# Kernel optimization log

Hardware: AMD Instinct MI355X
Metric: run time of the kernel (lower is better)

Reference implementation:

```python
import jax, jax.numpy as jnp
import numpy as np

IN_F = 4096
OUT_F = 4096
RANK = 32
GROUP = 64  # int4 weight quantization group size along in_features


def setup_inputs() -> dict:
    key = jax.random.key(0)
    k_x, k_w, k_s, k_ld, k_lu, k_b = jax.random.split(key, 6)
    x = jax.random.normal(k_x, (4096, IN_F), dtype=jnp.float32)
    # int4 weight codes in [-8, 7], stored as int32
    qweight = jax.random.randint(k_w, (OUT_F, IN_F), -8, 8, dtype=jnp.int32)
    # per-(out_channel, group) scales
    wscale = jax.random.uniform(k_s, (OUT_F, IN_F // GROUP), dtype=jnp.float32, minval=0.01, maxval=0.05)
    # low-rank SVD correction branch (LoRA-style)
    lora_down = jax.random.normal(k_ld, (RANK, IN_F), dtype=jnp.float32) * 0.02
    lora_up = jax.random.normal(k_lu, (OUT_F, RANK), dtype=jnp.float32) * 0.02
    bias = jax.random.normal(k_b, (OUT_F,), dtype=jnp.float32) * 0.01
    return {"x": x, "qweight": qweight, "wscale": wscale,
            "lora_down": lora_down, "lora_up": lora_up, "bias": bias}


def reference(x, qweight, wscale, lora_down, lora_up, bias):
    out_f, in_f = qweight.shape
    # dequantize int4 weights group-wise: W[o, g*G+i] = q * scale[o, g]
    W = (qweight.astype(jnp.float32).reshape(out_f, in_f // GROUP, GROUP)
         * wscale[:, :, None]).reshape(out_f, in_f)
    # per-token symmetric int4 activation quantization (W4A4 main path)
    ascale = jnp.maximum(jnp.max(jnp.abs(x), axis=-1, keepdims=True), 1e-6) / 7.0
    xq = jnp.clip(jnp.round(x / ascale), -8.0, 7.0) * ascale  # fake-quantized x
    # main quantized GEMM
    main = jnp.einsum('ti,oi->to', xq, W)
    # low-rank correction uses full-precision activations
    lora = jnp.einsum('tr,or->to', jnp.einsum('ti,ri->tr', x, lora_down), lora_up)
    return main + lora + bias[None, :]
```

## Files before the change

### kernel.cpp

```cpp
#include <hip/hip_runtime.h>

typedef __bf16 bf16x8 __attribute__((ext_vector_type(8)));
typedef float f32x4 __attribute__((ext_vector_type(4)));
typedef unsigned short u16;

#define IN_F 4096
#define OUT_F 4096
#define NTOK 4096
#define RANK 32
#define KEXT 4160
#define NT (KEXT / 64)
#define ROWB ((size_t)KEXT * 2)

__device__ __forceinline__ u16 f2bf(float f) {
  union { float f; unsigned u; } c; c.f = f;
  unsigned u = c.u;
  return (u16)((u + 0x7FFFu + ((u >> 16) & 1u)) >> 16);
}

__device__ __forceinline__ void gload_lds16(const void* g, void* l) {
  __builtin_amdgcn_global_load_lds((const __attribute__((address_space(1))) void*)g,
                                   (__attribute__((address_space(3))) void*)l,
                                   16, 0, 0);
}

__global__ __launch_bounds__(256) void prep_kernel(const float* __restrict__ x,
                                                   u16* __restrict__ A,
                                                   float* __restrict__ ascale) {
  int t = blockIdx.x;
  int tid = threadIdx.x;
  const float4* xr = (const float4*)(x + (size_t)t * IN_F);
  float4 v[4];
  float m = 0.f;
#pragma unroll
  for (int i = 0; i < 4; ++i) {
    v[i] = xr[tid + i * 256];
    m = fmaxf(m, fmaxf(fmaxf(fabsf(v[i].x), fabsf(v[i].y)),
                       fmaxf(fabsf(v[i].z), fabsf(v[i].w))));
  }
#pragma unroll
  for (int off = 32; off > 0; off >>= 1) m = fmaxf(m, __shfl_xor(m, off));
  __shared__ float wmax[4];
  if ((tid & 63) == 0) wmax[tid >> 6] = m;
  __syncthreads();
  m = fmaxf(fmaxf(wmax[0], wmax[1]), fmaxf(wmax[2], wmax[3]));
  float as = fmaxf(m, 1e-6f) / 7.f;
  float inv = 1.f / as;
  if (tid == 0) ascale[t] = as;
  u16* Ar = A + (size_t)t * KEXT;
#pragma unroll
  for (int i = 0; i < 4; ++i) {
    float q0 = fminf(fmaxf(rintf(v[i].x * inv), -8.f), 7.f);
    float q1 = fminf(fmaxf(rintf(v[i].y * inv), -8.f), 7.f);
    float q2 = fminf(fmaxf(rintf(v[i].z * inv), -8.f), 7.f);
    float q3 = fminf(fmaxf(rintf(v[i].w * inv), -8.f), 7.f);
    ushort4 u;
    u.x = f2bf(q0); u.y = f2bf(q1); u.z = f2bf(q2); u.w = f2bf(q3);
    *(ushort4*)(Ar + (size_t)(tid + i * 256) * 4) = u;
  }
  if (tid < 8) {
    ushort4 z; z.x = z.y = z.z = z.w = 0;
    *(ushort4*)(Ar + IN_F + 32 + tid * 4) = z;
  }
}

__global__ __launch_bounds__(256) void dequant_kernel(const int* __restrict__ qw,
                                                      const float* __restrict__ wscale,
                                                      const float* __restrict__ lu,
                                                      u16* __restrict__ B) {
  int o = blockIdx.x;
  int tid = threadIdx.x;
  const int4* qr = (const int4*)(qw + (size_t)o * IN_F);
  const float* sr = wscale + (size_t)o * (IN_F / 64);
  u16* Br = B + (size_t)o * KEXT;
#pragma unroll
  for (int s = 0; s < 4; ++s) {
    int e = tid + s * 256;
    int4 q = qr[e];
    float sc = sr[e >> 4];
    ushort4 u;
    u.x = f2bf((float)q.x * sc);
    u.y = f2bf((float)q.y * sc);
    u.z = f2bf((float)q.z * sc);
    u.w = f2bf((float)q.w * sc);
    *(ushort4*)(Br + (size_t)4 * e) = u;
  }
  if (tid < RANK) Br[IN_F + tid] = f2bf(lu[(size_t)o * RANK + tid]);
  if (tid < 8) {
    ushort4 z; z.x = z.y = z.z = z.w = 0;
    *(ushort4*)(Br + IN_F + 32 + tid * 4) = z;
  }
}

__global__ __launch_bounds__(256) void lorad_kernel(const float* __restrict__ x,
                                                    const float* __restrict__ ld,
                                                    float* __restrict__ tr8) {
  __shared__ float Xs[128][68];
  __shared__ float Ls[32][68];
  int b = blockIdx.x;
  int t0 = (b >> 3) * 128;
  int kbase = (b & 7) * 512;
  int tid = threadIdx.x;
  int rb = tid & 7;
  int tb = tid >> 3;
  float acc[4][4];
#pragma unroll
  for (int i = 0; i < 4; ++i)
#pragma unroll
    for (int j = 0; j < 4; ++j) acc[i][j] = 0.f;

  for (int kc = 0; kc < 512; kc += 64) {
    int k0 = kbase + kc;
    __syncthreads();
#pragma unroll
    for (int s = 0; s < 8; ++s) {
      int e = tid + s * 256;
      int row = e >> 4, c4 = (e & 15) * 4;
      float4 vv = *(const float4*)(x + (size_t)(t0 + row) * IN_F + k0 + c4);
      *(float4*)&Xs[row][c4] = vv;
    }
#pragma unroll
    for (int s = 0; s < 2; ++s) {
      int e = tid + s * 256;
      int row = e >> 4, c4 = (e & 15) * 4;
      float4 vv = *(const float4*)(ld + (size_t)row * IN_F + k0 + c4);
      *(float4*)&Ls[row][c4] = vv;
    }
    __syncthreads();
    for (int k4 = 0; k4 < 64; k4 += 4) {
      float4 lv[4], xv[4];
#pragma unroll
      for (int r = 0; r < 4; ++r) lv[r] = *(float4*)&Ls[rb + r * 8][k4];
#pragma unroll
      for (int mm = 0; mm < 4; ++mm) xv[mm] = *(float4*)&Xs[tb + mm * 32][k4];
#pragma unroll
      for (int mm = 0; mm < 4; ++mm)
#pragma unroll
        for (int r = 0; r < 4; ++r)
          acc[mm][r] += xv[mm].x * lv[r].x + xv[mm].y * lv[r].y +
                        xv[mm].z * lv[r].z + xv[mm].w * lv[r].w;
    }
  }
  float* dst = tr8 + (size_t)(b & 7) * NTOK * RANK;
#pragma unroll
  for (int mm = 0; mm < 4; ++mm)
#pragma unroll
    for (int r = 0; r < 4; ++r)
      dst[(size_t)(t0 + tb + mm * 32) * RANK + rb + r * 8] = acc[mm][r];
}

__global__ __launch_bounds__(256) void trwrite_kernel(const float* __restrict__ tr8,
                                                      const float* __restrict__ ascale,
                                                      u16* __restrict__ A) {
  int idx = blockIdx.x * 256 + threadIdx.x;
  int t = idx >> 5, r = idx & 31;
  float s = 0.f;
#pragma unroll
  for (int k = 0; k < 8; ++k) s += tr8[(size_t)k * NTOK * RANK + idx];
  A[(size_t)t * KEXT + IN_F + r] = f2bf(s / ascale[t]);
}


__device__ __forceinline__ void stage_tile(const char* g, char* ldst, int tid) {
#pragma unroll
  for (int h = 0; h < 4; ++h)
    gload_lds16(g + (size_t)h * (64 * ROWB), ldst + h * 8192 + tid * 16);
}

#define BARRIER() do { asm volatile("s_barrier" ::: "memory"); __builtin_amdgcn_sched_barrier(0); } while (0)

__global__ __launch_bounds__(512, 2) void gemm_kernel(const u16* __restrict__ A,
                                                      const u16* __restrict__ B,
                                                      const float* __restrict__ ascale,
                                                      const float* __restrict__ bias,
                                                      float* __restrict__ out) {
  __shared__ __align__(16) char smem[131072];
  int b = blockIdx.x;
  int swz = (b & 7) * 32 + (b >> 3);
  int by = swz >> 4, bx = swz & 15;
  int tm = by * 256, tn = bx * 256;
  int tid = threadIdx.x;
  int lane = tid & 63, wid = tid >> 6;
  int wr = wid >> 2, wc = wid & 3;
  int l15 = lane & 15, l4 = lane >> 4;
  int xorb = (l15 & 7) << 4;
  int colx0 = (l4 * 16) ^ xorb;
  int colx1 = (l4 * 16 + 64) ^ xorb;
  int a_base = wr * 16384 + l15 * 128;
  int b_base = wc * 8192 + l15 * 128;

  int r0 = tid >> 3;
  int cb = (((tid & 7) ^ ((tid >> 3) & 7)) << 4);
  const char* ag = (const char*)A + (size_t)(tm + r0) * ROWB + cb;
  const char* bg = (const char*)B + (size_t)(tn + r0) * ROWB + cb;

  f32x4 acc[8][4];
#pragma unroll
  for (int i = 0; i < 8; ++i)
#pragma unroll
    for (int j = 0; j < 4; ++j) acc[i][j] = (f32x4){0.f, 0.f, 0.f, 0.f};

  stage_tile(ag, smem, tid);
  stage_tile(bg, smem + 65536, tid);
  stage_tile(ag + 128, smem + 32768, tid);
  stage_tile(bg + 128, smem + 65536 + 32768, tid);
  asm volatile("s_waitcnt vmcnt(8)" ::: "memory");
  BARRIER();

  const char* apf = ag + 256;
  const char* bpf = bg + 256;
  bf16x8 af[8][2], bf[2][2];

  for (int t = 0; t < NT; ++t) {
    int c = t & 1;
    int ao = c * 32768 + a_base;
    int bo = 65536 + c * 32768 + b_base;
    bool pf = (t + 2) < NT;

#pragma unroll
    for (int i = 0; i < 4; ++i) {
      af[i][0] = *(const bf16x8*)(smem + ao + i * 2048 + colx0);
      af[i][1] = *(const bf16x8*)(smem + ao + i * 2048 + colx1);
    }
#pragma unroll
    for (int j = 0; j < 2; ++j) {
      bf[j][0] = *(const bf16x8*)(smem + bo + j * 2048 + colx0);
      bf[j][1] = *(const bf16x8*)(smem + bo + j * 2048 + colx1);
    }
    BARRIER();
    __builtin_amdgcn_s_setprio(1);
#pragma unroll
    for (int i = 0; i < 4; ++i)
#pragma unroll
      for (int j = 0; j < 2; ++j) {
        acc[i][j] = __builtin_amdgcn_mfma_f32_16x16x32_bf16(af[i][0], bf[j][0], acc[i][j], 0, 0, 0);
        acc[i][j] = __builtin_amdgcn_mfma_f32_16x16x32_bf16(af[i][1], bf[j][1], acc[i][j], 0, 0, 0);
      }
    __builtin_amdgcn_s_setprio(0);
    __builtin_amdgcn_sched_barrier(0);
    BARRIER();

#pragma unroll
    for (int i = 4; i < 8; ++i) {
      af[i][0] = *(const bf16x8*)(smem + ao + i * 2048 + colx0);
      af[i][1] = *(const bf16x8*)(smem + ao + i * 2048 + colx1);
    }
    BARRIER();
    __builtin_amdgcn_s_setprio(1);
#pragma unroll
    for (int i = 4; i < 8; ++i)
#pragma unroll
      for (int j = 0; j < 2; ++j) {
        acc[i][j] = __builtin_amdgcn_mfma_f32_16x16x32_bf16(af[i][0], bf[j][0], acc[i][j], 0, 0, 0);
        acc[i][j] = __builtin_amdgcn_mfma_f32_16x16x32_bf16(af[i][1], bf[j][1], acc[i][j], 0, 0, 0);
      }
    __builtin_amdgcn_s_setprio(0);
    __builtin_amdgcn_sched_barrier(0);
    BARRIER();

#pragma unroll
    for (int j = 0; j < 2; ++j) {
      bf[j][0] = *(const bf16x8*)(smem + bo + (j + 2) * 2048 + colx0);
      bf[j][1] = *(const bf16x8*)(smem + bo + (j + 2) * 2048 + colx1);
    }
    if (pf) stage_tile(apf, smem + c * 32768, tid);
    BARRIER();
    __builtin_amdgcn_s_setprio(1);
#pragma unroll
    for (int i = 0; i < 4; ++i)
#pragma unroll
      for (int j = 0; j < 2; ++j) {
        acc[i][j + 2] = __builtin_amdgcn_mfma_f32_16x16x32_bf16(af[i][0], bf[j][0], acc[i][j + 2], 0, 0, 0);
        acc[i][j + 2] = __builtin_amdgcn_mfma_f32_16x16x32_bf16(af[i][1], bf[j][1], acc[i][j + 2], 0, 0, 0);
      }
    __builtin_amdgcn_s_setprio(0);
    __builtin_amdgcn_sched_barrier(0);
    BARRIER();

    if (pf) {
      stage_tile(bpf, smem + 65536 + c * 32768, tid);
      asm volatile("s_waitcnt vmcnt(8)" ::: "memory");
    } else if (t == NT - 2) {
      asm volatile("s_waitcnt vmcnt(0)" ::: "memory");
    }
    BARRIER();
    __builtin_amdgcn_s_setprio(1);
#pragma unroll
    for (int i = 4; i < 8; ++i)
#pragma unroll
      for (int j = 0; j < 2; ++j) {
        acc[i][j + 2] = __builtin_amdgcn_mfma_f32_16x16x32_bf16(af[i][0], bf[j][0], acc[i][j + 2], 0, 0, 0);
        acc[i][j + 2] = __builtin_amdgcn_mfma_f32_16x16x32_bf16(af[i][1], bf[j][1], acc[i][j + 2], 0, 0, 0);
      }
    __builtin_amdgcn_s_setprio(0);
    __builtin_amdgcn_sched_barrier(0);
    BARRIER();

    apf += 128;
    bpf += 128;
  }

#pragma unroll
  for (int i = 0; i < 8; ++i) {
    int rowb = tm + wr * 128 + i * 16 + l4 * 4;
#pragma unroll
    for (int j = 0; j < 4; ++j) {
      int col = tn + wc * 64 + j * 16 + l15;
      float bv = bias[col];
#pragma unroll
      for (int q = 0; q < 4; ++q)
        out[(size_t)(rowb + q) * OUT_F + col] = acc[i][j][q] * ascale[rowb + q] + bv;
    }
  }
}

extern "C" void kernel_launch(void* const* d_in, const int* in_sizes, int n_in,
                              void* d_out, int out_size, void* d_ws, size_t ws_size,
                              hipStream_t stream) {
  const float* x = (const float*)d_in[0];
  const int* qw = (const int*)d_in[1];
  const float* wscale = (const float*)d_in[2];
  const float* ld = (const float*)d_in[3];
  const float* lu = (const float*)d_in[4];
  const float* bias = (const float*)d_in[5];
  float* out = (float*)d_out;

  char* ws = (char*)d_ws;
  const size_t szA = (size_t)NTOK * KEXT * sizeof(u16);
  const size_t szB = (size_t)OUT_F * KEXT * sizeof(u16);
  u16* Aext = (u16*)ws;
  u16* Bext = (u16*)(ws + szA);
  float* ascale = (float*)(ws + szA + szB);
  float* tr8 = (float*)(ws + szA + szB + 16384);

  prep_kernel<<<NTOK, 256, 0, stream>>>(x, Aext, ascale);
  dequant_kernel<<<OUT_F, 256, 0, stream>>>(qw, wscale, lu, Bext);
  lorad_kernel<<<256, 256, 0, stream>>>(x, ld, tr8);
  trwrite_kernel<<<NTOK * RANK / 256, 256, 0, stream>>>(tr8, ascale, Aext);
  gemm_kernel<<<(NTOK / 256) * (OUT_F / 256), 512, 0, stream>>>(Aext, Bext, ascale, bias, out);
}
```

Before: 194.0 us.

## Hoist all LDS fragment loads to iteration start and cut barriers per K-step

Each K-step now reads all A and B fragments from LDS at the start, holding 8x2 A and 4x2 B vectors, instead of interleaving four load phases between the MFMA blocks. This cuts the workgroup barriers per iteration from about eight to three, placed only where global-to-LDS prefetches need buffer reuse to be safe. The aim is to remove barrier stalls and let the LDS reads overlap with MFMA work. In exchange, more fragment registers are live at once, which adds register pressure under the 512-thread, 2-block launch bounds and could cause spills or lower occupancy.

```diff
diff --git a/kernel.cpp b/kernel.cpp
--- a/kernel.cpp
+++ b/kernel.cpp
@@ -167,7 +167,8 @@
     gload_lds16(g + (size_t)h * (64 * ROWB), ldst + h * 8192 + tid * 16);
 }
 
-#define BARRIER() do { asm volatile("s_barrier" ::: "memory"); __builtin_amdgcn_sched_barrier(0); } while (0)
+#define PIN_BARRIER() do { __builtin_amdgcn_sched_barrier(0); \
+                           asm volatile("s_barrier" ::: "memory"); } while (0)
 
 __global__ __launch_bounds__(512, 2) void gemm_kernel(const u16* __restrict__ A,
                                                       const u16* __restrict__ B,
@@ -205,11 +206,11 @@
   stage_tile(ag + 128, smem + 32768, tid);
   stage_tile(bg + 128, smem + 65536 + 32768, tid);
   asm volatile("s_waitcnt vmcnt(8)" ::: "memory");
-  BARRIER();
+  PIN_BARRIER();
 
   const char* apf = ag + 256;
   const char* bpf = bg + 256;
-  bf16x8 af[8][2], bf[2][2];
+  bf16x8 af[8][2], bf[4][2];
 
   for (int t = 0; t < NT; ++t) {
     int c = t & 1;
@@ -227,7 +228,17 @@
       bf[j][0] = *(const bf16x8*)(smem + bo + j * 2048 + colx0);
       bf[j][1] = *(const bf16x8*)(smem + bo + j * 2048 + colx1);
     }
-    BARRIER();
+#pragma unroll
+    for (int i = 4; i < 8; ++i) {
+      af[i][0] = *(const bf16x8*)(smem + ao + i * 2048 + colx0);
+      af[i][1] = *(const bf16x8*)(smem + ao + i * 2048 + colx1);
+    }
+#pragma unroll
+    for (int j = 2; j < 4; ++j) {
+      bf[j][0] = *(const bf16x8*)(smem + bo + j * 2048 + colx0);
+      bf[j][1] = *(const bf16x8*)(smem + bo + j * 2048 + colx1);
+    }
+
     __builtin_amdgcn_s_setprio(1);
 #pragma unroll
     for (int i = 0; i < 4; ++i)
@@ -237,15 +248,7 @@
         acc[i][j] = __builtin_amdgcn_mfma_f32_16x16x32_bf16(af[i][1], bf[j][1], acc[i][j], 0, 0, 0);
       }
     __builtin_amdgcn_s_setprio(0);
-    __builtin_amdgcn_sched_barrier(0);
-    BARRIER();
-
-#pragma unroll
-    for (int i = 4; i < 8; ++i) {
-      af[i][0] = *(const bf16x8*)(smem + ao + i * 2048 + colx0);
-      af[i][1] = *(const bf16x8*)(smem + ao + i * 2048 + colx1);
-    }
-    BARRIER();
+
     __builtin_amdgcn_s_setprio(1);
 #pragma unroll
     for (int i = 4; i < 8; ++i)
@@ -255,46 +258,36 @@
         acc[i][j] = __builtin_amdgcn_mfma_f32_16x16x32_bf16(af[i][1], bf[j][1], acc[i][j], 0, 0, 0);
       }
     __builtin_amdgcn_s_setprio(0);
-    __builtin_amdgcn_sched_barrier(0);
-    BARRIER();
-
-#pragma unroll
-    for (int j = 0; j < 2; ++j) {
-      bf[j][0] = *(const bf16x8*)(smem + bo + (j + 2) * 2048 + colx0);
-      bf[j][1] = *(const bf16x8*)(smem + bo + (j + 2) * 2048 + colx1);
-    }
+    PIN_BARRIER();
     if (pf) stage_tile(apf, smem + c * 32768, tid);
-    BARRIER();
+
     __builtin_amdgcn_s_setprio(1);
 #pragma unroll
     for (int i = 0; i < 4; ++i)
 #pragma unroll
-      for (int j = 0; j < 2; ++j) {
-        acc[i][j + 2] = __builtin_amdgcn_mfma_f32_16x16x32_bf16(af[i][0], bf[j][0], acc[i][j + 2], 0, 0, 0);
-        acc[i][j + 2] = __builtin_amdgcn_mfma_f32_16x16x32_bf16(af[i][1], bf[j][1], acc[i][j + 2], 0, 0, 0);
+      for (int j = 2; j < 4; ++j) {
+        acc[i][j] = __builtin_amdgcn_mfma_f32_16x16x32_bf16(af[i][0], bf[j][0], acc[i][j], 0, 0, 0);
+        acc[i][j] = __builtin_amdgcn_mfma_f32_16x16x32_bf16(af[i][1], bf[j][1], acc[i][j], 0, 0, 0);
       }
     __builtin_amdgcn_s_setprio(0);
-    __builtin_amdgcn_sched_barrier(0);
-    BARRIER();
-
+    PIN_BARRIER();
     if (pf) {
       stage_tile(bpf, smem + 65536 + c * 32768, tid);
       asm volatile("s_waitcnt vmcnt(8)" ::: "memory");
     } else if (t == NT - 2) {
       asm volatile("s_waitcnt vmcnt(0)" ::: "memory");
     }
-    BARRIER();
+
     __builtin_amdgcn_s_setprio(1);
 #pragma unroll
     for (int i = 4; i < 8; ++i)
 #pragma unroll
-      for (int j = 0; j < 2; ++j) {
-        acc[i][j + 2] = __builtin_amdgcn_mfma_f32_16x16x32_bf16(af[i][0], bf[j][0], acc[i][j + 2], 0, 0, 0);
-        acc[i][j + 2] = __builtin_amdgcn_mfma_f32_16x16x32_bf16(af[i][1], bf[j][1], acc[i][j + 2], 0, 0, 0);
+      for (int j = 2; j < 4; ++j) {
+        acc[i][j] = __builtin_amdgcn_mfma_f32_16x16x32_bf16(af[i][0], bf[j][0], acc[i][j], 0, 0, 0);
+        acc[i][j] = __builtin_amdgcn_mfma_f32_16x16x32_bf16(af[i][1], bf[j][1], acc[i][j], 0, 0, 0);
       }
     __builtin_amdgcn_s_setprio(0);
-    __builtin_amdgcn_sched_barrier(0);
-    BARRIER();
+    PIN_BARRIER();
 
     apf += 128;
     bpf += 128;
```

Measured after the change: 180.1 us. 1.08x faster.
